# Performance work log

Measured on AMD Instinct MI355X. Metric: run time of the kernel, lower is better.

Reference implementation:

```python
import jax, jax.numpy as jnp
import numpy as np

B, T, D = 2, 2048, 2048
H, HD = 16, 128            # num_heads, head_dim = D // H
DVH = 2                    # dynamic_value_num_heads
NVK = 4                    # num_v_keys = int(sqrt(H))
TOPK = DVH * 2             # = 4 <= NVK


def setup_inputs() -> dict:
    key = jax.random.key(0)
    ks = jax.random.split(key, 12)
    s = jnp.float32(0.02)
    return {
        "x": jax.random.normal(ks[0], (B, T, D), jnp.float32),
        "Wq": jax.random.normal(ks[1], (D, D), jnp.float32) * s,
        "bq": jnp.zeros((D,), jnp.float32),
        "Wk": jax.random.normal(ks[2], (D, D), jnp.float32) * s,
        "bk": jnp.zeros((D,), jnp.float32),
        "Wvq": jax.random.normal(ks[3], (HD * DVH, D), jnp.float32) * s,
        "bvq": jnp.zeros((HD * DVH,), jnp.float32),
        "v_keys": jax.random.normal(ks[4], (DVH, NVK, HD), jnp.float32) * s,
        "v_embed": jax.random.normal(ks[5], (H, HD * H), jnp.float32) * s,
        "Wo": jax.random.normal(ks[6], (D, D), jnp.float32) * s,
        "bo": jnp.zeros((D,), jnp.float32),
    }


def reference(x, Wq, bq, Wk, bk, Wvq, bvq, v_keys, v_embed, Wo, bo):
    b, t, d = x.shape
    # q/k projections -> [b, H, t, HD]
    q = (x @ Wq.T + bq).reshape(b, t, H, HD).transpose(0, 2, 1, 3)
    k = (x @ Wk.T + bk).reshape(b, t, H, HD).transpose(0, 2, 1, 3)

    # --- compute_value_states ---
    vq = (x @ Wvq.T + bvq).reshape(b, t, DVH, HD)          # [b,t,h,n]
    sim = jnp.einsum('bthn,hkn->bthk', vq, v_keys)         # [b,t,DVH,NVK]
    _, idx = jax.lax.top_k(sim, TOPK)                      # [b,t,DVH,TOPK]
    ve = v_embed[idx]                                      # gather -> [b,t,DVH,TOPK,d]
    # einsum 'btd,bthkd->btd' == x * sum over (h,k)
    vs = x * ve.sum(axis=(2, 3))                           # [b,t,d]
    v = vs.reshape(b, t, H, HD).transpose(0, 2, 1, 3)      # [b,H,t,HD]

    # --- hand-rolled causal attention ---
    scores = jnp.einsum('bhqd,bhkd->bhqk', q, k) / np.float32(np.sqrt(HD))
    min_val = jnp.finfo(x.dtype).min
    mask = jnp.triu(jnp.full((t, t), min_val, dtype=x.dtype), 1)
    scores = scores + mask
    w = jax.nn.softmax(scores.astype(jnp.float32), axis=-1).astype(x.dtype)
    o = jnp.einsum('bhqk,bhkd->bhqd', w, v)                # [b,H,t,HD]
    o = o.transpose(0, 2, 1, 3).reshape(b, t, d)
    return o @ Wo.T + bo
```

## Files before the change

### kernel.cpp

```cpp
#include <hip/hip_runtime.h>
#include <hip/hip_bf16.h>

#define DEV __device__ __forceinline__

typedef __bf16 bf16x8 __attribute__((ext_vector_type(8)));
typedef __bf16 bf16x4 __attribute__((ext_vector_type(4)));
typedef float f32x4 __attribute__((ext_vector_type(4)));

static constexpr int kB = 2, kT = 2048, kD = 2048, kH = 16, kHD = 128;
static constexpr int kBT = kB * kT;

#if __has_builtin(__builtin_amdgcn_exp2f)
DEV float fast_exp2(float x) { return __builtin_amdgcn_exp2f(x); }
#else
DEV float fast_exp2(float x) { return exp2f(x); }
#endif

DEV unsigned short f2bf(float f) {
  union { __hip_bfloat16 h; unsigned short u; } cv;
  cv.h = __float2bfloat16(f);
  return cv.u;
}

DEV void gl_lds16(const void* g, void* l) {
  __builtin_amdgcn_global_load_lds(
      (const __attribute__((address_space(1))) unsigned int*)g,
      (__attribute__((address_space(3))) unsigned int*)l, 16, 0, 0);
}

#define MFMA(a, b, c) __builtin_amdgcn_mfma_f32_16x16x32_bf16(a, b, c, 0, 0, 0)

DEV int swz4(int row) { return (row ^ (row >> 2)) & 3; }

__global__ __launch_bounds__(256) void prep_kernel(
    const float* __restrict__ x, const float* __restrict__ v_embed,
    const float* __restrict__ Wq, const float* __restrict__ Wk,
    const float* __restrict__ Wo, unsigned short* __restrict__ vt,
    unsigned short* __restrict__ xb, unsigned short* __restrict__ wqb,
    unsigned short* __restrict__ wkb, unsigned short* __restrict__ wob) {
  const int tid = threadIdx.x;
  const int bx = blockIdx.x;
  if (bx >= 1024) {
    const int j = bx - 1024;
    const int which = j >> 12;
    const int i = (j & 4095) * 256 + tid;
    const float* s = which == 0 ? Wq : which == 1 ? Wk : Wo;
    unsigned short* d = which == 0 ? wqb : which == 1 ? wkb : wob;
    float4 v = ((const float4*)s)[i];
    ushort4 o;
    o.x = f2bf(v.x); o.y = f2bf(v.y); o.z = f2bf(v.z); o.w = f2bf(v.w);
    ((ushort4*)d)[i] = o;
    return;
  }
  __shared__ __align__(16) unsigned short sT[128 * 72];
  const int t0 = (bx & 31) * 64, h = (bx >> 5) & 15, b = bx >> 9;
  const int d4 = tid & 31, r8 = tid >> 5;
  const int dg = h * kHD + d4 * 4;
  float4 e0 = *(const float4*)(v_embed + dg);
  float4 e1 = *(const float4*)(v_embed + kD + dg);
  float4 e2 = *(const float4*)(v_embed + 2 * kD + dg);
  float4 e3 = *(const float4*)(v_embed + 3 * kD + dg);
  float4 c4;
  c4.x = 2.f * (e0.x + e1.x + e2.x + e3.x);
  c4.y = 2.f * (e0.y + e1.y + e2.y + e3.y);
  c4.z = 2.f * (e0.z + e1.z + e2.z + e3.z);
  c4.w = 2.f * (e0.w + e1.w + e2.w + e3.w);
#pragma unroll
  for (int it = 0; it < 8; it++) {
    const int t = r8 + it * 8;
    const size_t row = (size_t)(b * kT + t0 + t) * kD + dg;
    float4 v = *(const float4*)(x + row);
    ushort4 xo;
    xo.x = f2bf(v.x); xo.y = f2bf(v.y); xo.z = f2bf(v.z); xo.w = f2bf(v.w);
    *(ushort4*)(xb + row) = xo;
    sT[(d4 * 4 + 0) * 72 + t] = f2bf(v.x * c4.x);
    sT[(d4 * 4 + 1) * 72 + t] = f2bf(v.y * c4.y);
    sT[(d4 * 4 + 2) * 72 + t] = f2bf(v.z * c4.z);
    sT[(d4 * 4 + 3) * 72 + t] = f2bf(v.w * c4.w);
  }
  __syncthreads();
#pragma unroll
  for (int it = 0; it < 4; it++) {
    const int hd = (tid >> 3) + it * 32;
    const int tt = (tid & 7) * 8;
    bf16x8 vv = *(const bf16x8*)(sT + hd * 72 + tt);
    *(bf16x8*)(vt + ((size_t)((b * kH + h) * kHD + hd)) * kT + t0 + tt) = vv;
  }
}

template <int NREP, bool BF16OUT, bool FUSED2>
__global__ __launch_bounds__(256, 4) void gemm_bt(
    const unsigned short* __restrict__ A, const unsigned short* __restrict__ B1,
    const unsigned short* __restrict__ B2, const float* __restrict__ bias1,
    const float* __restrict__ bias2, void* __restrict__ C1, void* __restrict__ C2,
    float scale1, float scale2) {
  constexpr int BN = NREP * 32;
  constexpr int N = kD, K = kD;
  __shared__ __align__(16) unsigned short As[2][128 * 32], Bs[2][BN * 32];
  int bxn, byn, bzn;
  if constexpr (FUSED2) {
    const int lb = blockIdx.x + (blockIdx.y << 4) + (blockIdx.z << 9);
    const int xcd = lb & 7, r = lb >> 3;
    bzn = xcd & 1;
    bxn = (((xcd >> 1) & 1) << 3) + (r & 7);
    byn = ((xcd >> 2) << 4) + (r >> 3);
  } else if constexpr (NREP == 2) {
    const int lb = blockIdx.x + (blockIdx.y << 5);
    const int xcd = lb & 7, r = lb >> 3;
    bzn = 0;
    bxn = ((xcd & 3) << 3) + (r & 7);
    byn = ((xcd >> 2) << 4) + (r >> 3);
  } else {
    const int lb = blockIdx.x + (blockIdx.y << 4);
    const int xcd = lb & 7, r = lb >> 3;
    bzn = 0;
    bxn = ((xcd & 1) << 3) + (r & 7);
    byn = ((xcd >> 1) << 3) + (r >> 3);
  }
  const unsigned short* Bm = (FUSED2 && bzn) ? B2 : B1;
  const float* bias = (FUSED2 && bzn) ? bias2 : bias1;
  void* Cout = (FUSED2 && bzn) ? C2 : C1;
  const float scale = (FUSED2 && bzn) ? scale2 : scale1;
  const int tid = threadIdx.x;
  const int lane = tid & 63, wave = tid >> 6;
  const int wr = wave >> 1, wc = wave & 1;
  const int m0 = byn * 128, n0 = bxn * BN;
  const int frow = lane & 15, fc = lane >> 4;

  f32x4 acc[4][NREP];
#pragma unroll
  for (int i = 0; i < 4; i++)
#pragma unroll
    for (int j = 0; j < NREP; j++)
#pragma unroll
      for (int r = 0; r < 4; r++) acc[i][j][r] = 0.f;

  const int r0 = tid >> 2, c0 = (tid & 3) ^ swz4(r0);
  const int p1 = tid + 256;
  const int r1 = p1 >> 2, c1 = (p1 & 3) ^ swz4(r1);

  const unsigned short* Ab = A + (size_t)m0 * K;
  const unsigned short* Bb = Bm + (size_t)n0 * K;

  for (int k0 = 0; k0 < K; k0 += 64) {
    __syncthreads();
#pragma unroll
    for (int hh = 0; hh < 2; hh++) {
      const int kk = k0 + hh * 32;
      gl_lds16(Ab + (size_t)r0 * K + kk + c0 * 8, &As[hh][tid * 8]);
      gl_lds16(Ab + (size_t)r1 * K + kk + c1 * 8, &As[hh][p1 * 8]);
      gl_lds16(Bb + (size_t)r0 * K + kk + c0 * 8, &Bs[hh][tid * 8]);
      if constexpr (NREP == 4)
        gl_lds16(Bb + (size_t)r1 * K + kk + c1 * 8, &Bs[hh][p1 * 8]);
    }
    __syncthreads();
#pragma unroll
    for (int hh = 0; hh < 2; hh++) {
      bf16x8 af[4], bfr[NREP];
#pragma unroll
      for (int mi = 0; mi < 4; mi++) {
        int row = wr * 64 + mi * 16 + frow;
        af[mi] = *(const bf16x8*)(&As[hh][(row * 4 + (fc ^ swz4(row))) * 8]);
      }
#pragma unroll
      for (int ni = 0; ni < NREP; ni++) {
        int row = wc * (NREP * 16) + ni * 16 + frow;
        bfr[ni] = *(const bf16x8*)(&Bs[hh][(row * 4 + (fc ^ swz4(row))) * 8]);
      }
#pragma unroll
      for (int mi = 0; mi < 4; mi++)
#pragma unroll
        for (int ni = 0; ni < NREP; ni++)
          acc[mi][ni] = MFMA(af[mi], bfr[ni], acc[mi][ni]);
    }
  }
#pragma unroll
  for (int ni = 0; ni < NREP; ni++) {
    const int n = n0 + wc * (NREP * 16) + ni * 16 + frow;
    const float bs = bias[n];
#pragma unroll
    for (int mi = 0; mi < 4; mi++) {
      const int mb = m0 + wr * 64 + mi * 16 + fc * 4;
#pragma unroll
      for (int r = 0; r < 4; r++) {
        const float v = (acc[mi][ni][r] + bs) * scale;
        if (BF16OUT)
          ((unsigned short*)Cout)[(size_t)(mb + r) * N + n] = f2bf(v);
        else
          ((float*)Cout)[(size_t)(mb + r) * N + n] = v;
      }
    }
  }
}

__global__ __launch_bounds__(256, 2) void attn2_kernel(
    const unsigned short* __restrict__ Q, const unsigned short* __restrict__ Kg,
    const unsigned short* __restrict__ Vt, unsigned short* __restrict__ O) {
  __shared__ __align__(16) unsigned short sK[2][64 * 128];
  __shared__ __align__(16) unsigned short sV[2][64 * 128];
  const int tid = threadIdx.x, l = tid & 63, w = tid >> 6;
  const int g = l >> 4, q15 = l & 15;
  const int bid = blockIdx.x;
  const int xcd = bid & 7, rest = bid >> 3;
  const int gidx = xcd + 8 * (rest & 3);
  const int pi = rest >> 2;
  const int h = gidx & 15, b = gidx >> 4;

  for (int half = 0; half < 2; half++) {
    const int qt = half == 0 ? (31 - pi) : pi;
    const int q0 = qt * 64;
    const int nkb = qt + 1;
    const int q = q0 + w * 16 + q15;

    __syncthreads();
    for (int i = 0; i < 4; i++) {
      const int idx = tid + i * 256;
      const int key = idx >> 4, cc = (idx & 15) ^ (key & 15);
      gl_lds16(Kg + (size_t)(b * kT + key) * kD + h * kHD + cc * 8,
               &sK[0][idx * 8]);
    }
    for (int i = 0; i < 4; i++) {
      const int idx = tid + i * 256;
      const int hd = idx >> 3;
      const int cc = (idx & 7) ^ (hd & 7) ^ (((hd >> 3) & 1) << 2);
      gl_lds16(Vt + ((size_t)((b * kH + h) * kHD + hd)) * kT + cc * 8,
               &sV[0][idx * 8]);
    }

    bf16x8 qf[4];
    const unsigned short* Qrow = Q + (size_t)(b * kT + q) * kD + h * kHD;
#pragma unroll
    for (int kk = 0; kk < 4; kk++)
      qf[kk] = *(const bf16x8*)(Qrow + kk * 32 + g * 8);

    f32x4 oacc[8];
#pragma unroll
    for (int ni = 0; ni < 8; ni++)
      for (int r = 0; r < 4; r++) oacc[ni][r] = 0.f;
    float m_i = -1e30f, l_i = 0.f;

    for (int kb = 0; kb < nkb; kb++) {
      const int bb = kb & 1;
      __syncthreads();
      if (kb + 1 < nkb) {
        const int k0n = (kb + 1) * 64;
        const int nb = 1 - bb;
#pragma unroll
        for (int i = 0; i < 4; i++) {
          const int idx = tid + i * 256;
          const int key = idx >> 4, cc = (idx & 15) ^ (key & 15);
          gl_lds16(Kg + (size_t)(b * kT + k0n + key) * kD + h * kHD + cc * 8,
                   &sK[nb][idx * 8]);
        }
#pragma unroll
        for (int i = 0; i < 4; i++) {
          const int idx = tid + i * 256;
          const int hd = idx >> 3;
          const int cc = (idx & 7) ^ (hd & 7) ^ (((hd >> 3) & 1) << 2);
          gl_lds16(Vt + ((size_t)((b * kH + h) * kHD + hd)) * kT + k0n + cc * 8,
                   &sV[nb][idx * 8]);
        }
      }

      f32x4 st[4];
#pragma unroll
      for (int s = 0; s < 4; s++)
        for (int r = 0; r < 4; r++) st[s][r] = 0.f;
#pragma unroll
      for (int s = 0; s < 4; s++) {
        const int key = s * 16 + q15;
#pragma unroll
        for (int kk = 0; kk < 4; kk++) {
          bf16x8 kf = *(const bf16x8*)(
              &sK[bb][(key * 16 + ((kk * 4 + g) ^ (key & 15))) * 8]);
          st[s] = MFMA(kf, qf[kk], st[s]);
        }
      }
      if (kb == nkb - 1) {
        const int k0 = kb * 64;
#pragma unroll
        for (int s = 0; s < 4; s++)
          for (int r = 0; r < 4; r++)
            if (k0 + s * 16 + g * 4 + r > q) st[s][r] = -1e30f;
      }
      float mx = -1e30f;
#pragma unroll
      for (int s = 0; s < 4; s++)
        for (int r = 0; r < 4; r++) mx = fmaxf(mx, st[s][r]);
      const bool defer = __all(mx - m_i <= 8.0f);
      float mn, alpha;
      if (defer) {
        mn = m_i;
        alpha = 1.f;
      } else {
        mx = fmaxf(mx, __shfl_xor(mx, 16, 64));
        mx = fmaxf(mx, __shfl_xor(mx, 32, 64));
        mn = fmaxf(m_i, mx);
        alpha = fast_exp2(m_i - mn);
      }
      float rs = 0.f;
      union { bf16x8 v; unsigned short u[8]; } pkv[2];
#pragma unroll
      for (int s = 0; s < 4; s++)
        for (int r = 0; r < 4; r++) {
          const float p = fast_exp2(st[s][r] - mn);
          rs += p;
          pkv[s >> 1].u[(s & 1) * 4 + r] = f2bf(p);
        }
      rs += __shfl_xor(rs, 16, 64);
      rs += __shfl_xor(rs, 32, 64);
      m_i = mn;
      l_i = l_i * alpha + rs;
      if (!defer) {
#pragma unroll
        for (int ni = 0; ni < 8; ni++)
          for (int r = 0; r < 4; r++) oacc[ni][r] *= alpha;
      }
#pragma unroll
      for (int ni = 0; ni < 8; ni++) {
        const int hd = ni * 16 + q15;
        const int hx = (hd & 7) ^ (((hd >> 3) & 1) << 2), base = hd * 8;
#pragma unroll
        for (int c = 0; c < 2; c++) {
          const int c4l = 8 * c + g;
          const int c4h = 8 * c + 4 + g;
          bf16x4 lo = *(const bf16x4*)(
              &sV[bb][(base + ((c4l >> 1) ^ hx)) * 8 + (c4l & 1) * 4]);
          bf16x4 hi = *(const bf16x4*)(
              &sV[bb][(base + ((c4h >> 1) ^ hx)) * 8 + (c4h & 1) * 4]);
          bf16x8 vf = __builtin_shufflevector(lo, hi, 0, 1, 2, 3, 4, 5, 6, 7);
          oacc[ni] = MFMA(vf, pkv[c].v, oacc[ni]);
        }
      }
    }
    const float inv = 1.f / l_i;
    unsigned short* Orow = O + (size_t)(b * kT + q) * kD + h * kHD;
#pragma unroll
    for (int ni = 0; ni < 8; ni++) {
      ushort4 o4;
      o4.x = f2bf(oacc[ni][0] * inv);
      o4.y = f2bf(oacc[ni][1] * inv);
      o4.z = f2bf(oacc[ni][2] * inv);
      o4.w = f2bf(oacc[ni][3] * inv);
      *(ushort4*)(Orow + ni * 16 + g * 4) = o4;
    }
  }
}

extern "C" void kernel_launch(void* const* d_in, const int* in_sizes, int n_in,
                              void* d_out, int out_size, void* d_ws, size_t ws_size,
                              hipStream_t stream) {
  const float* x       = (const float*)d_in[0];
  const float* Wq      = (const float*)d_in[1];
  const float* bq      = (const float*)d_in[2];
  const float* Wk      = (const float*)d_in[3];
  const float* bk      = (const float*)d_in[4];
  const float* v_embed = (const float*)d_in[8];
  const float* Wo      = (const float*)d_in[9];
  const float* bo      = (const float*)d_in[10];
  float* out = (float*)d_out;

  char* w = (char*)d_ws;
  unsigned short* xb  = (unsigned short*)w; w += (size_t)kBT * kD * 2;
  unsigned short* qb  = (unsigned short*)w; w += (size_t)kBT * kD * 2;
  unsigned short* kb  = (unsigned short*)w; w += (size_t)kBT * kD * 2;
  unsigned short* ob  = (unsigned short*)w; w += (size_t)kBT * kD * 2;
  unsigned short* vtb = (unsigned short*)w; w += (size_t)kBT * kD * 2;
  unsigned short* wqb = (unsigned short*)w; w += (size_t)kD * kD * 2;
  unsigned short* wkb = (unsigned short*)w; w += (size_t)kD * kD * 2;
  unsigned short* wob = (unsigned short*)w; w += (size_t)kD * kD * 2;

  prep_kernel<<<dim3(1024 + 3 * 4096), 256, 0, stream>>>(
      x, v_embed, Wq, Wk, Wo, vtb, xb, wqb, wkb, wob);

  const float scaleQ = 0.08838834764831845f * 1.4426950408889634f;
  gemm_bt<4, true, true><<<dim3(kD / 128, kBT / 128, 2), 256, 0, stream>>>(
      xb, wqb, wkb, bq, bk, qb, kb, scaleQ, 1.0f);

  attn2_kernel<<<dim3(512), 256, 0, stream>>>(qb, kb, vtb, ob);

  gemm_bt<4, false, false><<<dim3(kD / 128, kBT / 128, 1), 256, 0, stream>>>(
      ob, wob, nullptr, bo, nullptr, out, nullptr, 1.0f, 1.0f);
}
```

Measured before the change: 316.4 us.

## Add 256x256 eight-wave GEMM with 4-stage pipeline for fused Q/K projection

Replaces the 128x128-tile fused Q/K projection GEMM with a new kernel that uses 256x256 tiles, 512 threads (8 waves), and a 4-deep LDS ring buffer for global-to-LDS prefetch. The MFMA work is split into two phases per k-step, with barriers and priority hints placed so LDS reads and global loads overlap with matrix math. The larger tile raises data reuse per byte loaded but uses 128KB of LDS and yields only 256 blocks, which may limit occupancy and tail balance. An unused NREP==2 tile-mapping branch is also removed.

```diff
diff --git a/kernel.cpp b/kernel.cpp
--- a/kernel.cpp
+++ b/kernel.cpp
@@ -88,6 +88,138 @@
   }
 }
 
+__global__ __launch_bounds__(512, 2) void gemm8p_qk(
+    const unsigned short* __restrict__ A, const unsigned short* __restrict__ B1,
+    const unsigned short* __restrict__ B2, const float* __restrict__ bias1,
+    const float* __restrict__ bias2, unsigned short* __restrict__ C1,
+    unsigned short* __restrict__ C2, float scale1, float scale2) {
+  constexpr int N = kD, K = kD;
+  constexpr int NT = K / 32;
+  __shared__ __align__(16) unsigned short As[4][256 * 32];
+  __shared__ __align__(16) unsigned short Bs[4][256 * 32];
+  const int lb = blockIdx.x + (blockIdx.y << 3) + (blockIdx.z << 7);
+  const int xcd = lb & 7, r2 = lb >> 3;
+  const int bzn = xcd & 1;
+  const int byn = ((xcd >> 1) << 2) + (r2 >> 3);
+  const int bxn = r2 & 7;
+  const unsigned short* Bm = bzn ? B2 : B1;
+  const float* bias = bzn ? bias2 : bias1;
+  unsigned short* Cout = bzn ? C2 : C1;
+  const float scale = bzn ? scale2 : scale1;
+
+  const int tid = threadIdx.x;
+  const int lane = tid & 63, wave = tid >> 6;
+  const int wr = wave >> 2, wc = wave & 3;
+  const int m0 = byn * 256, n0 = bxn * 256;
+  const int frow = lane & 15, fc = lane >> 4;
+
+  f32x4 acc[8][4];
+#pragma unroll
+  for (int i = 0; i < 8; i++)
+#pragma unroll
+    for (int j = 0; j < 4; j++)
+#pragma unroll
+      for (int r = 0; r < 4; r++) acc[i][j][r] = 0.f;
+
+  const int q0 = tid, q1 = tid + 512;
+  const int r0 = q0 >> 2, c0 = (q0 & 3) ^ swz4(r0);
+  const int r1 = q1 >> 2, c1 = (q1 & 3) ^ swz4(r1);
+
+  const unsigned short* Ab = A + (size_t)m0 * K;
+  const unsigned short* Bb = Bm + (size_t)n0 * K;
+
+  auto stA = [&](int bf, int k0) {
+    gl_lds16(Ab + (size_t)r0 * K + k0 + c0 * 8, &As[bf][q0 * 8]);
+    gl_lds16(Ab + (size_t)r1 * K + k0 + c1 * 8, &As[bf][q1 * 8]);
+  };
+  auto stB = [&](int bf, int k0) {
+    gl_lds16(Bb + (size_t)r0 * K + k0 + c0 * 8, &Bs[bf][q0 * 8]);
+    gl_lds16(Bb + (size_t)r1 * K + k0 + c1 * 8, &Bs[bf][q1 * 8]);
+  };
+
+  stA(0, 0); stB(0, 0);
+  stA(1, 32); stB(1, 32);
+  stA(2, 64); stB(2, 64);
+  asm volatile("s_waitcnt vmcnt(8)" ::: "memory");
+  __builtin_amdgcn_s_barrier();
+  __builtin_amdgcn_sched_barrier(0);
+
+  for (int k = 0; k < NT; ++k) {
+    const int buf = k & 3;
+    const int nbuf = (k + 3) & 3;
+    const int kn = (k + 3) * 32;
+    const bool pre = (k + 3) < NT;
+    const unsigned short* Asb = As[buf];
+    const unsigned short* Bsb = Bs[buf];
+
+    bf16x8 bfr[4], af[4];
+#pragma unroll
+    for (int ni = 0; ni < 4; ni++) {
+      const int row = wc * 64 + ni * 16 + frow;
+      bfr[ni] = *(const bf16x8*)(Bsb + (row * 4 + (fc ^ swz4(row))) * 8);
+    }
+#pragma unroll
+    for (int mi = 0; mi < 4; mi++) {
+      const int row = wr * 128 + mi * 16 + frow;
+      af[mi] = *(const bf16x8*)(Asb + (row * 4 + (fc ^ swz4(row))) * 8);
+    }
+    if (pre) stA(nbuf, kn);
+    __builtin_amdgcn_s_barrier();
+    asm volatile("s_waitcnt lgkmcnt(0)" ::: "memory");
+    __builtin_amdgcn_sched_barrier(0);
+    __builtin_amdgcn_s_setprio(1);
+#pragma unroll
+    for (int mi = 0; mi < 4; mi++)
+#pragma unroll
+      for (int ni = 0; ni < 4; ni++)
+        acc[mi][ni] = MFMA(af[mi], bfr[ni], acc[mi][ni]);
+    __builtin_amdgcn_s_setprio(0);
+    __builtin_amdgcn_s_barrier();
+    __builtin_amdgcn_sched_barrier(0);
+
+    bf16x8 af2[4];
+#pragma unroll
+    for (int mi = 0; mi < 4; mi++) {
+      const int row = wr * 128 + (mi + 4) * 16 + frow;
+      af2[mi] = *(const bf16x8*)(Asb + (row * 4 + (fc ^ swz4(row))) * 8);
+    }
+    if (pre) stB(nbuf, kn);
+    if (k < NT - 3)
+      asm volatile("s_waitcnt vmcnt(8)" ::: "memory");
+    else if (k == NT - 3)
+      asm volatile("s_waitcnt vmcnt(4)" ::: "memory");
+    else if (k == NT - 2)
+      asm volatile("s_waitcnt vmcnt(0)" ::: "memory");
+    __builtin_amdgcn_s_barrier();
+    asm volatile("s_waitcnt lgkmcnt(0)" ::: "memory");
+    __builtin_amdgcn_sched_barrier(0);
+    __builtin_amdgcn_s_setprio(1);
+#pragma unroll
+    for (int mi = 0; mi < 4; mi++)
+#pragma unroll
+      for (int ni = 0; ni < 4; ni++)
+        acc[mi + 4][ni] = MFMA(af2[mi], bfr[ni], acc[mi + 4][ni]);
+    __builtin_amdgcn_s_setprio(0);
+    __builtin_amdgcn_s_barrier();
+    __builtin_amdgcn_sched_barrier(0);
+  }
+
+#pragma unroll
+  for (int ni = 0; ni < 4; ni++) {
+    const int n = n0 + wc * 64 + ni * 16 + frow;
+    const float bs = bias[n];
+#pragma unroll
+    for (int mi = 0; mi < 8; mi++) {
+      const int mb = m0 + wr * 128 + mi * 16 + fc * 4;
+#pragma unroll
+      for (int r = 0; r < 4; r++) {
+        const float v = (acc[mi][ni][r] + bs) * scale;
+        Cout[(size_t)(mb + r) * N + n] = f2bf(v);
+      }
+    }
+  }
+}
+
 template <int NREP, bool BF16OUT, bool FUSED2>
 __global__ __launch_bounds__(256, 4) void gemm_bt(
     const unsigned short* __restrict__ A, const unsigned short* __restrict__ B1,
@@ -104,12 +236,6 @@
     bzn = xcd & 1;
     bxn = (((xcd >> 1) & 1) << 3) + (r & 7);
     byn = ((xcd >> 2) << 4) + (r >> 3);
-  } else if constexpr (NREP == 2) {
-    const int lb = blockIdx.x + (blockIdx.y << 5);
-    const int xcd = lb & 7, r = lb >> 3;
-    bzn = 0;
-    bxn = ((xcd & 3) << 3) + (r & 7);
-    byn = ((xcd >> 2) << 4) + (r >> 3);
   } else {
     const int lb = blockIdx.x + (blockIdx.y << 4);
     const int xcd = lb & 7, r = lb >> 3;
@@ -374,7 +500,7 @@
       x, v_embed, Wq, Wk, Wo, vtb, xb, wqb, wkb, wob);
 
   const float scaleQ = 0.08838834764831845f * 1.4426950408889634f;
-  gemm_bt<4, true, true><<<dim3(kD / 128, kBT / 128, 2), 256, 0, stream>>>(
+  gemm8p_qk<<<dim3(kD / 256, kBT / 256, 2), 512, 0, stream>>>(
       xb, wqb, wkb, bq, bk, qb, kb, scaleQ, 1.0f);
 
   attn2_kernel<<<dim3(512), 256, 0, stream>>>(qb, kb, vtb, ob);
```

Result: faster. 308.8 us (-2.4%).
